# Kernel optimization log

Hardware: AMD Instinct MI355X
Metric: run time of the kernel (lower is better)

Reference implementation:

```python
import jax, jax.numpy as jnp
import numpy as np

BS, SEQ, ENC, DEC, HEADS, INTERM = 32, 2048, 512, 512, 8, 128
IH = INTERM * HEADS


def setup_inputs() -> dict:
    key = jax.random.key(0)
    ks = jax.random.split(key, 16)
    s = 0.02
    return {
        "enc": jax.random.normal(ks[0], (BS, SEQ, ENC), jnp.float32),
        "dec": jax.random.normal(ks[1], (BS, 1, DEC + ENC), jnp.float32),
        "kappa": jax.random.uniform(ks[2], (BS, 1, HEADS), jnp.float32),
        "mask": jnp.ones((BS, SEQ, 1), jnp.float32),
        "Wv": jax.random.normal(ks[3], (ENC, IH), jnp.float32) * s,
        "bv": jnp.zeros((IH,), jnp.float32),
        "Wq": jax.random.normal(ks[4], (DEC + ENC, IH), jnp.float32) * s,
        "bq": jnp.zeros((IH,), jnp.float32),
        "Wf": jax.random.normal(ks[5], (IH, HEADS), jnp.float32) * s,
        "bf": jnp.zeros((HEADS,), jnp.float32),
        "Wb": jax.random.normal(ks[6], (DEC + ENC, HEADS), jnp.float32) * s,
        "bb": jnp.zeros((HEADS,), jnp.float32),
        "Wk": jax.random.normal(ks[7], (DEC + ENC, HEADS), jnp.float32) * s,
        "bk": jnp.zeros((HEADS,), jnp.float32),
        "Wfc": jax.random.normal(ks[8], (ENC * HEADS, ENC), jnp.float32) * s,
        "bfc": jnp.zeros((ENC,), jnp.float32),
    }


def reference(enc, dec, kappa, mask, Wv, bv, Wq, bq, Wf, bf, Wb, bb, Wk, bk, Wfc, bfc):
    bs, seq_len, _ = enc.shape
    sp = jax.nn.softplus
    value = enc @ Wv + bv                      # (bs, seq, IH)
    query = dec @ Wq + bq                      # (bs, 1, IH), broadcasts over seq
    alpha = sp(jnp.tanh(query + value) @ Wf + bf) * mask   # (bs, seq, heads)
    beta = sp(dec @ Wb + bb)                   # (bs, 1, heads)
    kappa = kappa + sp(dec @ Wk + bk)          # (bs, 1, heads)
    u = jnp.arange(seq_len, dtype=enc.dtype)[None, :, None]
    score = alpha * jnp.exp(-beta * (kappa - u) ** 2)       # (bs, seq, heads)
    # weighted reduction over seq: (bs, heads, enc) then flatten in heads-major order
    context = jnp.einsum("bsh,bse->bhe", score, enc).reshape(bs, -1)
    context = context @ Wfc + bfc              # (bs, enc)
    return context[:, None, :], kappa, score
```

## Files before the change

### kernel.cpp

```cpp
#include <hip/hip_runtime.h>
#include <cstdint>
#include <cstddef>

#define BSZ    32
#define SEQL   2048
#define ENCD   512
#define DE     1024
#define NHEADS 8
#define IHD    1024

typedef unsigned short u16;
typedef __bf16 bf16x8 __attribute__((ext_vector_type(8)));
typedef float floatx4 __attribute__((ext_vector_type(4)));
typedef unsigned short u16x8 __attribute__((ext_vector_type(8)));

__device__ __forceinline__ u16 f2bf(float f) {
    unsigned int u = __float_as_uint(f);
    u = (u + 0x7FFFu + ((u >> 16) & 1u)) >> 16;
    return (u16)u;
}
__device__ __forceinline__ float bf2f(u16 v) {
    return __uint_as_float(((unsigned int)v) << 16);
}
__device__ __forceinline__ float softplus_f(float x) {
    return fmaxf(x, 0.0f) + log1pf(__expf(-fabsf(x)));
}
__device__ __forceinline__ float tanh_fast(float x) {
    const float e = __expf(2.0f * x);
    return 1.0f - 2.0f / (e + 1.0f);
}
__device__ __forceinline__ void async_cp16(u16* lds, const u16* g) {
    __builtin_amdgcn_global_load_lds(
        (const __attribute__((address_space(1))) unsigned int*)g,
        (__attribute__((address_space(3))) unsigned int*)lds, 16, 0, 0);
}

__global__ __launch_bounds__(256) void pre_kernel(
    const float* __restrict__ Wv, const float* __restrict__ Wf,
    u16* __restrict__ WvT, u16* __restrict__ wfb,
    const float* __restrict__ dec, const float* __restrict__ kappa_in,
    const float* __restrict__ Wq, const float* __restrict__ bq,
    const float* __restrict__ bv,
    const float* __restrict__ Wb, const float* __restrict__ bb,
    const float* __restrict__ Wk, const float* __restrict__ bk,
    float* __restrict__ query_ws, float* __restrict__ beta_ws,
    float* __restrict__ kappa_out)
{
    __shared__ float sh[64 * 65];
    const int bid = blockIdx.x, tid = threadIdx.x;

    if (bid < 128) {
        const int nt = bid & 15, kt = bid >> 4;
        for (int i = tid; i < 4096; i += 256) {
            const int kk = i >> 6, nn = i & 63;
            sh[kk * 65 + nn] = Wv[(size_t)(kt * 64 + kk) * IHD + nt * 64 + nn];
        }
        __syncthreads();
        for (int i = tid; i < 4096; i += 256) {
            const int nn = i >> 6, kk = i & 63;
            WvT[(size_t)(nt * 64 + nn) * 512 + kt * 64 + kk] = f2bf(sh[kk * 65 + nn]);
        }
        return;
    }
    if (bid == 128) {
        for (int i = tid; i < 8192; i += 256) {
            const int j   = i & 7;
            const int fr8 = (i >> 3) & 7;
            const int qd  = (i >> 6) & 3;
            const int ks  = (i >> 8) & 3;
            const int nn  = i >> 10;
            const int row = nn * 128 + ks * 32 + qd * 8 + j;
            wfb[i] = f2bf(Wf[row * NHEADS + fr8]);
        }
        return;
    }
    const int p = bid - 129;
    const int b = p & 31, y = p >> 5;
    float* s_dec = sh;
    float* s_red = sh + DE;
    for (int i = tid; i < DE; i += 256) s_dec[i] = dec[b * DE + i];
    __syncthreads();

    if (y < 32) {
        const int cl = tid & 31, kg = tid >> 5;
        const int col = y * 32 + cl;
        float a = 0.f;
        const float* w = Wq + col;
        #pragma unroll 4
        for (int k = kg * 128; k < kg * 128 + 128; ++k)
            a = fmaf(s_dec[k], w[(size_t)k * IHD], a);
        s_red[tid] = a;
        __syncthreads();
        if (tid < 32) {
            float s = 0.f;
            #pragma unroll
            for (int i = 0; i < 8; ++i) s += s_red[i * 32 + tid];
            query_ws[(size_t)b * IHD + col] = s + bq[col] + bv[col];
        }
    } else {
        const int h = tid & 7, kg = tid >> 3;
        float ab = 0.f, ak = 0.f;
        for (int k = kg * 32; k < kg * 32 + 32; ++k) {
            const float d = s_dec[k];
            ab = fmaf(d, Wb[k * NHEADS + h], ab);
            ak = fmaf(d, Wk[k * NHEADS + h], ak);
        }
        s_red[tid] = ab;
        __syncthreads();
        for (int off = 128; off >= 8; off >>= 1) {
            if (tid < off) s_red[tid] += s_red[tid + off];
            __syncthreads();
        }
        const float abT = (tid < 8) ? s_red[tid] : 0.f;
        __syncthreads();
        s_red[tid] = ak;
        __syncthreads();
        for (int off = 128; off >= 8; off >>= 1) {
            if (tid < off) s_red[tid] += s_red[tid + off];
            __syncthreads();
        }
        if (tid < 8) {
            beta_ws[b * NHEADS + tid]   = softplus_f(bb[tid] + abT);
            kappa_out[b * NHEADS + tid] = kappa_in[b * NHEADS + tid]
                                        + softplus_f(bk[tid] + s_red[tid]);
        }
    }
}

#define BM 128

__global__ __launch_bounds__(256, 2) void gemm_score_ctx_kernel(
    const float* __restrict__ enc, u16* __restrict__ encb,
    const u16* __restrict__ wvT,
    const u16* __restrict__ wfb2, const float* __restrict__ bf_g,
    const float* __restrict__ mask, const float* __restrict__ query_ws,
    const float* __restrict__ beta_ws, const float* __restrict__ kappa_out,
    float* __restrict__ score_out, float* __restrict__ ctx_part)
{
    __shared__ __align__(16) unsigned char smem[69632];
    u16*   tT      = (u16*)(smem + 32768);
    float* s_score = (float*)(smem + 65536);

    const int tid  = threadIdx.x;
    const int m0   = blockIdx.x * BM;
    const int b    = blockIdx.x >> 4;
    const int sc   = blockIdx.x & 15;
    const int lane = tid & 63;
    const int w    = tid >> 6;
    const int wr   = w >> 1, wc = w & 1;
    const int fr   = lane & 15, quad = lane >> 4;

    {
        const float4* src = (const float4*)enc + (size_t)m0 * 128;
        u16x8* dst = (u16x8*)(encb + (size_t)m0 * 512);
        for (int i = tid; i < 8192; i += 256) {
            const float4 a = src[i * 2], b2 = src[i * 2 + 1];
            u16x8 o;
            o[0] = f2bf(a.x);  o[1] = f2bf(a.y);  o[2] = f2bf(a.z);  o[3] = f2bf(a.w);
            o[4] = f2bf(b2.x); o[5] = f2bf(b2.y); o[6] = f2bf(b2.z); o[7] = f2bf(b2.w);
            dst[i] = o;
        }
        asm volatile("s_waitcnt vmcnt(0)" ::: "memory");
        __builtin_amdgcn_sched_barrier(0);
        __builtin_amdgcn_s_barrier();
    }

    int mA[4], csA[4];
    #pragma unroll
    for (int r = 0; r < 4; ++r) {
        const int c = r * 256 + tid;
        mA[r]  = c >> 3;
        csA[r] = (c & 7) ^ (mA[r] & 7);
    }

    auto stage = [&](int bufsel, int it) {
        u16* Ab = (u16*)(smem + bufsel * 32768);
        u16* Bb = Ab + 8192;
        const int nn2 = it >> 3, kt2 = it & 7;
        const size_t aoff = (size_t)kt2 * 64;
        const size_t boff = (size_t)nn2 * (128 * 512) + (size_t)kt2 * 64;
        #pragma unroll
        for (int r = 0; r < 4; ++r) {
            async_cp16(Ab + (r * 256 + (tid & 192)) * 8,
                       encb + (size_t)(m0 + mA[r]) * 512 + aoff + csA[r] * 8);
            async_cp16(Bb + (size_t)(r * 256 + (tid & 192)) * 8,
                       wvT + (size_t)mA[r] * 512 + boff + csA[r] * 8);
        }
    };

    floatx4 acc2[2] = {};

    stage(0, 0);

    for (int nn = 0; nn < 8; ++nn) {
        const int n0 = nn * 128;
        float qv[4];
        bf16x8 wfr[4];
        floatx4 acc[4][4] = {};

        #pragma unroll
        for (int kt = 0; kt < 8; ++kt) {
            const int it = nn * 8 + kt;
            if (kt < 7 || nn < 7)
                stage((it + 1) & 1, it + 1);
            if (kt == 0) {
                #pragma unroll
                for (int nt = 0; nt < 4; ++nt)
                    qv[nt] = query_ws[(size_t)b * IHD + n0 + wc * 64 + nt * 16 + fr];
                #pragma unroll
                for (int ks = 0; ks < 4; ++ks)
                    wfr[ks] = *(const bf16x8*)&wfb2[((nn * 4 + ks) * 4 + quad) * 64
                                                    + (fr & 7) * 8];
            }
            if (kt == 7 && nn == 7) {
                asm volatile("s_waitcnt vmcnt(0)" ::: "memory");
            } else if (kt == 0) {
                asm volatile("s_waitcnt vmcnt(16)" ::: "memory");
            } else {
                asm volatile("s_waitcnt vmcnt(8)" ::: "memory");
            }
            __builtin_amdgcn_sched_barrier(0);
            __builtin_amdgcn_s_barrier();

            u16* Ab = (u16*)(smem + (it & 1) * 32768);
            u16* Bb = Ab + 8192;
            __builtin_amdgcn_s_setprio(1);
            #pragma unroll
            for (int s2 = 0; s2 < 2; ++s2) {
                bf16x8 af[4], bfr[4];
                #pragma unroll
                for (int mt = 0; mt < 4; ++mt) {
                    const int ma = wr * 64 + mt * 16 + fr;
                    const int ca = (s2 * 4 + quad) ^ (ma & 7);
                    af[mt] = *(const bf16x8*)&Ab[ma * 64 + ca * 8];
                }
                #pragma unroll
                for (int nt = 0; nt < 4; ++nt) {
                    const int nb = wc * 64 + nt * 16 + fr;
                    const int cb = (s2 * 4 + quad) ^ (nb & 7);
                    bfr[nt] = *(const bf16x8*)&Bb[nb * 64 + cb * 8];
                }
                #pragma unroll
                for (int mt = 0; mt < 4; ++mt)
                    #pragma unroll
                    for (int nt = 0; nt < 4; ++nt)
                        acc[mt][nt] = __builtin_amdgcn_mfma_f32_16x16x32_bf16(
                            af[mt], bfr[nt], acc[mt][nt], 0, 0, 0);
            }
            __builtin_amdgcn_s_setprio(0);
            __builtin_amdgcn_sched_barrier(0);
            __builtin_amdgcn_s_barrier();
        }

        #pragma unroll
        for (int mt = 0; mt < 4; ++mt) {
            #pragma unroll
            for (int nt = 0; nt < 4; ++nt) {
                const int col = wc * 64 + nt * 16 + fr;
                #pragma unroll
                for (int reg = 0; reg < 4; ++reg) {
                    const int row = wr * 64 + mt * 16 + quad * 4 + reg;
                    ((__bf16*)tT)[row * 128 + (col ^ ((row & 7) << 3))] =
                        (__bf16)tanh_fast(acc[mt][nt][reg] + qv[nt]);
                }
            }
        }
        asm volatile("s_waitcnt lgkmcnt(0)" ::: "memory");
        __builtin_amdgcn_sched_barrier(0);
        __builtin_amdgcn_s_barrier();

        #pragma unroll
        for (int t = 0; t < 2; ++t) {
            const int row = w * 32 + t * 16 + fr;
            #pragma unroll
            for (int ks = 0; ks < 4; ++ks) {
                const bf16x8 ta = *(const bf16x8*)
                    &tT[row * 128 + ((ks * 32 + quad * 8) ^ ((row & 7) << 3))];
                acc2[t] = __builtin_amdgcn_mfma_f32_16x16x32_bf16(ta, wfr[ks], acc2[t], 0, 0, 0);
            }
        }
        __builtin_amdgcn_sched_barrier(0);
        __builtin_amdgcn_s_barrier();
    }

    if (fr < NHEADS) {
        const float bfh = bf_g[fr];
        const float bet = beta_ws[b * NHEADS + fr];
        const float kap = kappa_out[b * NHEADS + fr];
        #pragma unroll
        for (int t = 0; t < 2; ++t) {
            #pragma unroll
            for (int reg = 0; reg < 4; ++reg) {
                const int row  = w * 32 + t * 16 + quad * 4 + reg;
                const int grow = m0 + row;
                const int s = grow & 2047;
                const float alpha = softplus_f(acc2[t][reg] + bfh) * mask[grow];
                const float du = kap - (float)s;
                const float v = alpha * __expf(-bet * du * du);
                score_out[(size_t)grow * NHEADS + fr] = v;
                s_score[row * NHEADS + fr] = v;
            }
        }
    }
    asm volatile("s_waitcnt lgkmcnt(0)" ::: "memory");
    __builtin_amdgcn_s_barrier();

    {
        float acc0[8] = {}, acc1[8] = {};
        const u16* ep = encb + (size_t)m0 * 512 + lane * 8;
        #pragma unroll 4
        for (int s = 0; s < 128; ++s) {
            const u16x8 ev = *(const u16x8*)(ep + (size_t)s * 512);
            const float2 sc2 = *(const float2*)&s_score[s * NHEADS + 2 * w];
            #pragma unroll
            for (int j = 0; j < 8; ++j) {
                const float e = bf2f(ev[j]);
                acc0[j] = fmaf(sc2.x, e, acc0[j]);
                acc1[j] = fmaf(sc2.y, e, acc1[j]);
            }
        }
        const int e8 = lane * 8;
        float* outp = ctx_part + ((size_t)sc * BSZ + b) * (NHEADS * ENCD);
        *(float4*)&outp[(2 * w + 0) * ENCD + e8]     = make_float4(acc0[0], acc0[1], acc0[2], acc0[3]);
        *(float4*)&outp[(2 * w + 0) * ENCD + e8 + 4] = make_float4(acc0[4], acc0[5], acc0[6], acc0[7]);
        *(float4*)&outp[(2 * w + 1) * ENCD + e8]     = make_float4(acc1[0], acc1[1], acc1[2], acc1[3]);
        *(float4*)&outp[(2 * w + 1) * ENCD + e8 + 4] = make_float4(acc1[4], acc1[5], acc1[6], acc1[7]);
    }
}

__global__ __launch_bounds__(256) void ctx_reduce_kernel(
    const float* __restrict__ part, float* __restrict__ ctx_ws)
{
    const int i = blockIdx.x * 256 + threadIdx.x;
    float a = 0.f;
    #pragma unroll
    for (int sc = 0; sc < 16; ++sc)
        a += part[(size_t)sc * 131072 + i];
    ctx_ws[i] = a;
}

__global__ __launch_bounds__(256) void final_kernel(
    const float* __restrict__ ctx_ws, const float* __restrict__ Wfc,
    const float* __restrict__ bfc, float* __restrict__ out_ctx)
{
    __shared__ float s_ctx[32][128];
    const int jc = blockIdx.x, ks = blockIdx.y, tid = threadIdx.x;
    const int jl = tid & 31, bg = tid >> 5;
    const int j = jc * 32 + jl;
    const int k0 = ks * 128;

    for (int i = tid; i < 32 * 128; i += 256) {
        const int bb2 = i >> 7, kk = i & 127;
        s_ctx[bb2][kk] = ctx_ws[(size_t)bb2 * (NHEADS * ENCD) + k0 + kk];
    }
    __syncthreads();

    float a0 = 0.f, a1 = 0.f, a2 = 0.f, a3 = 0.f;
    for (int kk = 0; kk < 128; ++kk) {
        const float wv = Wfc[(size_t)(k0 + kk) * ENCD + j];
        a0 = fmaf(s_ctx[bg * 4 + 0][kk], wv, a0);
        a1 = fmaf(s_ctx[bg * 4 + 1][kk], wv, a1);
        a2 = fmaf(s_ctx[bg * 4 + 2][kk], wv, a2);
        a3 = fmaf(s_ctx[bg * 4 + 3][kk], wv, a3);
    }
    const float bias = (ks == 0) ? bfc[j] : 0.0f;
    atomicAdd(&out_ctx[(bg * 4 + 0) * ENCD + j], a0 + bias);
    atomicAdd(&out_ctx[(bg * 4 + 1) * ENCD + j], a1 + bias);
    atomicAdd(&out_ctx[(bg * 4 + 2) * ENCD + j], a2 + bias);
    atomicAdd(&out_ctx[(bg * 4 + 3) * ENCD + j], a3 + bias);
}

extern "C" void kernel_launch(void* const* d_in, const int* in_sizes, int n_in,
                              void* d_out, int out_size, void* d_ws, size_t ws_size,
                              hipStream_t stream)
{
    const float* enc   = (const float*)d_in[0];
    const float* dec   = (const float*)d_in[1];
    const float* kapin = (const float*)d_in[2];
    const float* mask  = (const float*)d_in[3];
    const float* Wv    = (const float*)d_in[4];
    const float* bv    = (const float*)d_in[5];
    const float* Wq    = (const float*)d_in[6];
    const float* bq    = (const float*)d_in[7];
    const float* Wf    = (const float*)d_in[8];
    const float* bf    = (const float*)d_in[9];
    const float* Wb    = (const float*)d_in[10];
    const float* bb    = (const float*)d_in[11];
    const float* Wk    = (const float*)d_in[12];
    const float* bk    = (const float*)d_in[13];
    const float* Wfc   = (const float*)d_in[14];
    const float* bfc   = (const float*)d_in[15];

    float* out       = (float*)d_out;
    float* out_ctx   = out;
    float* out_kappa = out + 16384;
    float* out_score = out + 16640;

    char* w = (char*)d_ws;
    u16*   enc_bf   = (u16*)w;
    float* ctx_part = (float*)(w + 67108864);
    u16*   wvT      = (u16*)(w + 75497472);
    float* q_ws     = (float*)(w + 76546048);
    float* beta_ws  = (float*)(w + 76677120);
    float* ctx_ws   = (float*)(w + 76678144);
    u16*   wfb      = (u16*)(w + 77202432);

    hipMemsetAsync(out_ctx, 0, 16384 * sizeof(float), stream);

    pre_kernel<<<dim3(128 + 1 + 1056), dim3(256), 0, stream>>>(
        Wv, Wf, wvT, wfb,
        dec, kapin, Wq, bq, bv, Wb, bb, Wk, bk, q_ws, beta_ws, out_kappa);

    gemm_score_ctx_kernel<<<dim3((BSZ * SEQL) / BM), dim3(256), 0, stream>>>(
        enc, enc_bf, wvT, wfb, bf, mask, q_ws, beta_ws, out_kappa,
        out_score, ctx_part);

    ctx_reduce_kernel<<<dim3(512), dim3(256), 0, stream>>>(ctx_part, ctx_ws);

    final_kernel<<<dim3(16, 32), dim3(256), 0, stream>>>(
        ctx_ws, Wfc, bfc, out_ctx);
}
```

Measured before the change: 398.1 us.

## Store enc tile in MFMA fragment order and load A operands directly from global

During conversion, the bf16 copy of the enc tile is written in MFMA fragment-major order. Each wave can then load its A fragments straight from global memory into registers, double-buffered across k-steps, and only the Wv B tile is staged through LDS. This cuts LDS traffic and halves the shared staging footprint. One trailing barrier per head-tile iteration is dropped, and the context reduction now reads the fp32 enc directly instead of the bf16 copy. The costs are scattered global reads during conversion, more registers for the prefetched A fragments, and twice the bytes read in the context pass.

```diff
diff --git a/kernel.cpp b/kernel.cpp
--- a/kernel.cpp
+++ b/kernel.cpp
@@ -151,10 +151,17 @@
     const int fr   = lane & 15, quad = lane >> 4;
 
     {
-        const float4* src = (const float4*)enc + (size_t)m0 * 128;
         u16x8* dst = (u16x8*)(encb + (size_t)m0 * 512);
         for (int i = tid; i < 8192; i += 256) {
-            const float4 a = src[i * 2], b2 = src[i * 2 + 1];
+            const int ln  = i & 63;
+            const int s2_ = (i >> 6) & 1;
+            const int mt_ = (i >> 7) & 3;
+            const int wr_ = (i >> 9) & 1;
+            const int kt_ = i >> 10;
+            const int row = wr_ * 64 + mt_ * 16 + (ln & 15);
+            const int col = kt_ * 64 + s2_ * 32 + (ln >> 4) * 8;
+            const float4* src = (const float4*)(enc + (size_t)(m0 + row) * 512 + col);
+            const float4 a = src[0], b2 = src[1];
             u16x8 o;
             o[0] = f2bf(a.x);  o[1] = f2bf(a.y);  o[2] = f2bf(a.z);  o[3] = f2bf(a.w);
             o[4] = f2bf(b2.x); o[5] = f2bf(b2.y); o[6] = f2bf(b2.z); o[7] = f2bf(b2.w);
@@ -165,92 +172,101 @@
         __builtin_amdgcn_s_barrier();
     }
 
-    int mA[4], csA[4];
+    const bf16x8* fragp = (const bf16x8*)(encb + (size_t)m0 * 512);
+
+    int mB[4], csB[4];
     #pragma unroll
     for (int r = 0; r < 4; ++r) {
         const int c = r * 256 + tid;
-        mA[r]  = c >> 3;
-        csA[r] = (c & 7) ^ (mA[r] & 7);
-    }
-
-    auto stage = [&](int bufsel, int it) {
-        u16* Ab = (u16*)(smem + bufsel * 32768);
-        u16* Bb = Ab + 8192;
-        const int nn2 = it >> 3, kt2 = it & 7;
-        const size_t aoff = (size_t)kt2 * 64;
-        const size_t boff = (size_t)nn2 * (128 * 512) + (size_t)kt2 * 64;
-        #pragma unroll
-        for (int r = 0; r < 4; ++r) {
-            async_cp16(Ab + (r * 256 + (tid & 192)) * 8,
-                       encb + (size_t)(m0 + mA[r]) * 512 + aoff + csA[r] * 8);
-            async_cp16(Bb + (size_t)(r * 256 + (tid & 192)) * 8,
-                       wvT + (size_t)mA[r] * 512 + boff + csA[r] * 8);
-        }
+        mB[r]  = c >> 3;
+        csB[r] = (c & 7) ^ (mB[r] & 7);
+    }
+
+    auto stageB = [&](int sel, int nn2, int kt2) {
+        u16* Bb = (u16*)(smem + sel * 16384);
+        const u16* src = wvT + (size_t)nn2 * 65536 + (size_t)kt2 * 64;
+        #pragma unroll
+        for (int r = 0; r < 4; ++r)
+            async_cp16(Bb + (r * 256 + (tid & 192)) * 8,
+                       src + (size_t)mB[r] * 512 + csB[r] * 8);
     };
 
+#define LOADA(DST, KT2)                                                        \
+    _Pragma("unroll")                                                          \
+    for (int mt_ = 0; mt_ < 4; ++mt_) {                                        \
+        _Pragma("unroll")                                                      \
+        for (int s2_ = 0; s2_ < 2; ++s2_)                                      \
+            DST[mt_][s2_] = fragp[(((KT2) * 2 + wr) * 8 + mt_ * 2 + s2_) * 64  \
+                                  + lane];                                     \
+    }
+
+#define KT_STEP(KT, AUSE, ALOAD)                                               \
+    {                                                                          \
+        if ((KT) < 7)      { stageB(((KT) + 1) & 1, nn, (KT) + 1);             \
+                             LOADA(ALOAD, (KT) + 1) }                          \
+        else if (nn < 7)   { stageB(0, nn + 1, 0);                             \
+                             LOADA(ALOAD, 0) }                                 \
+        if ((KT) == 7 && nn == 7) {                                            \
+            asm volatile("s_waitcnt vmcnt(0)" ::: "memory");                   \
+        } else {                                                               \
+            asm volatile("s_waitcnt vmcnt(12)" ::: "memory");                  \
+        }                                                                      \
+        __builtin_amdgcn_sched_barrier(0);                                     \
+        __builtin_amdgcn_s_barrier();     \
+        {                                                                      \
+            const u16* Bb_ = (const u16*)(smem + ((KT) & 1) * 16384);          \
+            __builtin_amdgcn_s_setprio(1);                                     \
+            _Pragma("unroll")                                                  \
+            for (int s2_ = 0; s2_ < 2; ++s2_) {                                \
+                bf16x8 bfr[4];                                                 \
+                _Pragma("unroll")                                              \
+                for (int nt_ = 0; nt_ < 4; ++nt_) {                            \
+                    const int nb_ = wc * 64 + nt_ * 16 + fr;                   \
+                    const int cb_ = (s2_ * 4 + quad) ^ (nb_ & 7);              \
+                    bfr[nt_] = *(const bf16x8*)&Bb_[nb_ * 64 + cb_ * 8];       \
+                }                                                              \
+                _Pragma("unroll")                                              \
+                for (int mt_ = 0; mt_ < 4; ++mt_) {                            \
+                    _Pragma("unroll")                                          \
+                    for (int nt_ = 0; nt_ < 4; ++nt_)                          \
+                        acc[mt_][nt_] = __builtin_amdgcn_mfma_f32_16x16x32_bf16( \
+                            AUSE[mt_][s2_], bfr[nt_], acc[mt_][nt_], 0, 0, 0); \
+                }                                                              \
+            }                                                                  \
+            __builtin_amdgcn_s_setprio(0);                                     \
+        }                                                                      \
+        __builtin_amdgcn_sched_barrier(0);                                     \
+        __builtin_amdgcn_s_barrier();     \
+    }
+
     floatx4 acc2[2] = {};
-
-    stage(0, 0);
+    bf16x8 afp0[4][2], afp1[4][2];
+
+    stageB(0, 0, 0);
+    LOADA(afp0, 0)
 
     for (int nn = 0; nn < 8; ++nn) {
         const int n0 = nn * 128;
+        floatx4 acc[4][4] = {};
+
+        KT_STEP(0, afp0, afp1)
+        KT_STEP(1, afp1, afp0)
+        KT_STEP(2, afp0, afp1)
+        KT_STEP(3, afp1, afp0)
+        KT_STEP(4, afp0, afp1)
+        KT_STEP(5, afp1, afp0)
+        KT_STEP(6, afp0, afp1)
+        KT_STEP(7, afp1, afp0)
+
         float qv[4];
         bf16x8 wfr[4];
-        floatx4 acc[4][4] = {};
-
-        #pragma unroll
-        for (int kt = 0; kt < 8; ++kt) {
-            const int it = nn * 8 + kt;
-            if (kt < 7 || nn < 7)
-                stage((it + 1) & 1, it + 1);
-            if (kt == 0) {
-                #pragma unroll
-                for (int nt = 0; nt < 4; ++nt)
-                    qv[nt] = query_ws[(size_t)b * IHD + n0 + wc * 64 + nt * 16 + fr];
-                #pragma unroll
-                for (int ks = 0; ks < 4; ++ks)
-                    wfr[ks] = *(const bf16x8*)&wfb2[((nn * 4 + ks) * 4 + quad) * 64
-                                                    + (fr & 7) * 8];
-            }
-            if (kt == 7 && nn == 7) {
-                asm volatile("s_waitcnt vmcnt(0)" ::: "memory");
-            } else if (kt == 0) {
-                asm volatile("s_waitcnt vmcnt(16)" ::: "memory");
-            } else {
-                asm volatile("s_waitcnt vmcnt(8)" ::: "memory");
-            }
-            __builtin_amdgcn_sched_barrier(0);
-            __builtin_amdgcn_s_barrier();
-
-            u16* Ab = (u16*)(smem + (it & 1) * 32768);
-            u16* Bb = Ab + 8192;
-            __builtin_amdgcn_s_setprio(1);
-            #pragma unroll
-            for (int s2 = 0; s2 < 2; ++s2) {
-                bf16x8 af[4], bfr[4];
-                #pragma unroll
-                for (int mt = 0; mt < 4; ++mt) {
-                    const int ma = wr * 64 + mt * 16 + fr;
-                    const int ca = (s2 * 4 + quad) ^ (ma & 7);
-                    af[mt] = *(const bf16x8*)&Ab[ma * 64 + ca * 8];
-                }
-                #pragma unroll
-                for (int nt = 0; nt < 4; ++nt) {
-                    const int nb = wc * 64 + nt * 16 + fr;
-                    const int cb = (s2 * 4 + quad) ^ (nb & 7);
-                    bfr[nt] = *(const bf16x8*)&Bb[nb * 64 + cb * 8];
-                }
-                #pragma unroll
-                for (int mt = 0; mt < 4; ++mt)
-                    #pragma unroll
-                    for (int nt = 0; nt < 4; ++nt)
-                        acc[mt][nt] = __builtin_amdgcn_mfma_f32_16x16x32_bf16(
-                            af[mt], bfr[nt], acc[mt][nt], 0, 0, 0);
-            }
-            __builtin_amdgcn_s_setprio(0);
-            __builtin_amdgcn_sched_barrier(0);
-            __builtin_amdgcn_s_barrier();
-        }
+        #pragma unroll
+        for (int nt = 0; nt < 4; ++nt)
+            qv[nt] = query_ws[(size_t)b * IHD + n0 + wc * 64 + nt * 16 + fr];
+        #pragma unroll
+        for (int ks = 0; ks < 4; ++ks)
+            wfr[ks] = *(const bf16x8*)&wfb2[((nn * 4 + ks) * 4 + quad) * 64
+                                            + (fr & 7) * 8];
 
         #pragma unroll
         for (int mt = 0; mt < 4; ++mt) {
@@ -279,8 +295,6 @@
                 acc2[t] = __builtin_amdgcn_mfma_f32_16x16x32_bf16(ta, wfr[ks], acc2[t], 0, 0, 0);
             }
         }
-        __builtin_amdgcn_sched_barrier(0);
-        __builtin_amdgcn_s_barrier();
     }
 
     if (fr < NHEADS) {
@@ -307,16 +321,17 @@
 
     {
         float acc0[8] = {}, acc1[8] = {};
-        const u16* ep = encb + (size_t)m0 * 512 + lane * 8;
+        const float* ep = enc + (size_t)m0 * 512 + lane * 8;
         #pragma unroll 4
         for (int s = 0; s < 128; ++s) {
-            const u16x8 ev = *(const u16x8*)(ep + (size_t)s * 512);
+            const float4 e0 = *(const float4*)(ep + (size_t)s * 512);
+            const float4 e1 = *(const float4*)(ep + (size_t)s * 512 + 4);
             const float2 sc2 = *(const float2*)&s_score[s * NHEADS + 2 * w];
+            const float ev[8] = {e0.x, e0.y, e0.z, e0.w, e1.x, e1.y, e1.z, e1.w};
             #pragma unroll
             for (int j = 0; j < 8; ++j) {
-                const float e = bf2f(ev[j]);
-                acc0[j] = fmaf(sc2.x, e, acc0[j]);
-                acc1[j] = fmaf(sc2.y, e, acc1[j]);
+                acc0[j] = fmaf(sc2.x, ev[j], acc0[j]);
+                acc1[j] = fmaf(sc2.y, ev[j], acc1[j]);
             }
         }
         const int e8 = lane * 8;
```

Result: slower. 565.7 us (+42.1%).
